# Optimization experiments

Measured on AMD Instinct MI355X. Metric: run time of the kernel, lower is better.

## Reference

```python
import jax, jax.numpy as jnp
import numpy as np

D = 512
NH = 8
DH = D // NH
B, L = 16, 1024


def setup_inputs() -> dict:
    key = jax.random.key(0)
    k1, k2, k3, k4 = jax.random.split(key, 4)
    queries = jax.random.normal(k1, (B, D, L), dtype=jnp.float32)
    mask = jax.random.randint(k2, (B, L), 0, 2, dtype=jnp.int32)
    # xavier-ish scale for 1x1 conv weights [out, in]
    w_mem = jax.random.normal(k3, (2 * D, D), dtype=jnp.float32) * (1.0 / np.sqrt(D))
    w_q = jax.random.normal(k4, (D, D), dtype=jnp.float32) * (1.0 / np.sqrt(D))
    return {"queries": queries, "mask": mask, "w_mem": w_mem, "w_q": w_q}


def _split_heads(x):
    # [B, L, D] -> [B, NH, L, DH]
    b, l, _ = x.shape
    return x.reshape(b, l, NH, DH).transpose(0, 2, 1, 3)


def reference(queries, mask, w_mem, w_q):
    # queries: [B, D, L] channels-first (1x1 Conv1d == per-position matmul)
    x = queries.transpose(0, 2, 1)                       # [B, L, D]
    mem = jnp.einsum('bld,ed->ble', x, w_mem)            # [B, L, 2D]
    qry = jnp.einsum('bld,ed->ble', x, w_q)              # [B, L, D]
    q = _split_heads(qry) * (DH ** -0.5)                 # [B, NH, L, DH]
    k = _split_heads(mem[..., :D])
    v = _split_heads(mem[..., D:])
    logits = jnp.einsum('bhqd,bhkd->bhqk', q, k)         # [B, NH, L, L]
    maskf = mask.astype(jnp.float32)[:, None, None, :]   # [B,1,1,L]
    logits = logits + (-1e30) * (1.0 - maskf)
    weights = jax.nn.softmax(logits, axis=-1)
    out = jnp.einsum('bhqk,bhkd->bhqd', weights, v)      # [B, NH, L, DH]
    out = out.transpose(0, 2, 1, 3).reshape(B, L, D)     # combine heads
    return out.transpose(0, 2, 1)                        # [B, D, L]
```

## Files before the change

kernel.cpp:

```cpp
#include <hip/hip_runtime.h>
#include <hip/hip_bf16.h>
#include <stdint.h>

#define Bsz 16
#define NHn 8
#define Dm  512
#define DHd 64
#define Ls  1024

typedef __attribute__((ext_vector_type(8))) short bf16x8;
typedef __attribute__((ext_vector_type(4))) float f32x4;
typedef __attribute__((ext_vector_type(16))) float f32x16;
typedef __attribute__((ext_vector_type(4))) unsigned int u32x4;

#define MFMA16 __builtin_amdgcn_mfma_f32_16x16x32_bf16
#define MFMA32 __builtin_amdgcn_mfma_f32_32x32x16_bf16

#define QSCALE 0.18033688011112042f

static __device__ __forceinline__ unsigned short f2bf(float f) {
    unsigned int u = __builtin_bit_cast(unsigned int, f);
    u += 0x7FFFu + ((u >> 16) & 1u);
    return (unsigned short)(u >> 16);
}

static __device__ __forceinline__ void gl2lds16(const void* g, void* l) {
    __builtin_amdgcn_global_load_lds(
        (const __attribute__((address_space(1))) unsigned int*)g,
        (__attribute__((address_space(3))) unsigned int*)l, 16, 0, 0);
}

__global__ void __launch_bounds__(256) pack_x(const float* __restrict__ q,
                                              unsigned short* __restrict__ X) {
    __shared__ float tile[64][68];
    const int bid = blockIdx.x;
    const int b  = bid >> 7;
    const int dt = (bid >> 4) & 7;
    const int lt = bid & 15;
    const int t  = threadIdx.x;
    const int tr = t >> 4;
    const int tc = (t & 15) * 4;
    const float* src = q + ((size_t)b * Dm + dt * 64) * Ls + lt * 64;
#pragma unroll
    for (int p = 0; p < 4; ++p) {
        const int r = p * 16 + tr;
        const float4 v = *(const float4*)(src + (size_t)r * Ls + tc);
        tile[r][tc+0] = v.x; tile[r][tc+1] = v.y; tile[r][tc+2] = v.z; tile[r][tc+3] = v.w;
    }
    __syncthreads();
    unsigned short* dst = X + (size_t)(b * Ls + lt * 64) * Dm + dt * 64;
#pragma unroll
    for (int p = 0; p < 4; ++p) {
        const int lr = p * 16 + tr;
        ushort4 o;
        o.x = f2bf(tile[tc+0][lr]);
        o.y = f2bf(tile[tc+1][lr]);
        o.z = f2bf(tile[tc+2][lr]);
        o.w = f2bf(tile[tc+3][lr]);
        *(ushort4*)(dst + (size_t)lr * Dm + tc) = o;
    }
}

__global__ void __launch_bounds__(256) pack_w(const float* __restrict__ wm,
                                              const float* __restrict__ wq,
                                              unsigned short* __restrict__ W) {
    const int i = (blockIdx.x * 256 + threadIdx.x) * 4;
    const int n = i >> 9;
    const int k = i & 511;
    const float* src = (n < 512) ? (wq + (size_t)n * 512 + k)
                                 : (wm + (size_t)(n - 512) * 512 + k);
    const float4 v = *(const float4*)src;
    ushort4 o;
    o.x = f2bf(v.x); o.y = f2bf(v.y); o.z = f2bf(v.z); o.w = f2bf(v.w);
    *(ushort4*)(W + i) = o;
}

__global__ void __launch_bounds__(256) gemm_qkv(const unsigned short* __restrict__ X,
                                                const unsigned short* __restrict__ W,
                                                unsigned short* __restrict__ Qb,
                                                unsigned short* __restrict__ Kb,
                                                unsigned short* __restrict__ VT) {
    __shared__ unsigned short Alds[2][128 * 64];
    __shared__ unsigned short Blds[2][128 * 64];
    const int bid = (blockIdx.x & 7) * 192 + (blockIdx.x >> 3);
    const int nt = bid % 12, mt = bid / 12;
    const int m0 = mt * 128, n0 = nt * 128;
    const int t = threadIdx.x;
    const int w = t >> 6, lane = t & 63, g = lane >> 4, c = lane & 15;
    const int wm = w >> 1, wn = w & 1;
    const int lrow = lane >> 3;
    const int scol = ((lane & 7) ^ lrow) * 8;

    const f32x4 fzero = {0.f, 0.f, 0.f, 0.f};
    f32x4 acc[4][4];
#pragma unroll
    for (int i = 0; i < 4; ++i)
#pragma unroll
        for (int j = 0; j < 4; ++j) acc[i][j] = fzero;

#define STAGE(BUF, KT) do {                                                      \
        const int k0_ = (KT) * 64;                                               \
        _Pragma("unroll")                                                        \
        for (int i_ = 0; i_ < 4; ++i_) {                                         \
            const int r0_ = w * 32 + i_ * 8;                                     \
            gl2lds16(X + (size_t)(m0 + r0_ + lrow) * Dm + k0_ + scol,            \
                     &Alds[BUF][r0_ * 64]);                                      \
            gl2lds16(W + (size_t)(n0 + r0_ + lrow) * Dm + k0_ + scol,            \
                     &Blds[BUF][r0_ * 64]);                                      \
        }                                                                        \
    } while (0)

#define KLOOP(SWAPPED) do {                                                      \
    for (int kt = 0; kt < 8; ++kt) {                                             \
        const int buf = kt & 1;                                                  \
        if (kt < 7) {                                                            \
            STAGE(buf ^ 1, kt + 1);                                              \
            asm volatile("s_waitcnt vmcnt(8)" ::: "memory");                     \
        } else {                                                                 \
            asm volatile("s_waitcnt vmcnt(0)" ::: "memory");                     \
        }                                                                        \
        __syncthreads();                                                         \
        const char* Ab = (const char*)&Alds[buf][0];                             \
        const char* Bb = (const char*)&Blds[buf][0];                             \
        _Pragma("unroll")                                                        \
        for (int kk = 0; kk < 2; ++kk) {                                         \
            bf16x8 av[4], bv[4];                                                 \
            _Pragma("unroll")                                                    \
            for (int mi = 0; mi < 4; ++mi) {                                     \
                const int R = wm * 64 + mi * 16 + c;                             \
                av[mi] = *(const bf16x8*)(Ab + R * 128 +                         \
                          ((kk * 64 + g * 16) ^ ((R & 7) << 4)));                \
            }                                                                    \
            _Pragma("unroll")                                                    \
            for (int nj = 0; nj < 4; ++nj) {                                     \
                const int R = wn * 64 + nj * 16 + c;                             \
                bv[nj] = *(const bf16x8*)(Bb + R * 128 +                         \
                          ((kk * 64 + g * 16) ^ ((R & 7) << 4)));                \
            }                                                                    \
            _Pragma("unroll")                                                    \
            for (int mi = 0; mi < 4; ++mi)                                       \
                _Pragma("unroll")                                                \
                for (int nj = 0; nj < 4; ++nj)                                   \
                    acc[mi][nj] = (SWAPPED)                                      \
                        ? MFMA16(bv[nj], av[mi], acc[mi][nj], 0, 0, 0)           \
                        : MFMA16(av[mi], bv[nj], acc[mi][nj], 0, 0, 0);          \
        }                                                                        \
        __syncthreads();                                                         \
    }                                                                            \
} while (0)

    STAGE(0, 0);
    const int bq = m0 >> 10;

    if (n0 < 1024) {
        KLOOP(1);
        const int m_loc = (m0 & 1023) + wm * 64 + c;
        const int hbase = ((n0 < 512) ? n0 : (n0 - 512)) >> 6;
        unsigned short* dstbase = (n0 < 512) ? Qb : Kb;
        const float scale = (n0 < 512) ? QSCALE : 1.0f;
        unsigned short* base = dstbase + ((size_t)(bq * NHn + hbase + wn) * Ls) * DHd;
        const int dh0 = g * 4;
#pragma unroll
        for (int nj = 0; nj < 4; ++nj) {
#pragma unroll
            for (int mi = 0; mi < 4; ++mi) {
                ushort4 o;
                o.x = f2bf(acc[mi][nj][0] * scale);
                o.y = f2bf(acc[mi][nj][1] * scale);
                o.z = f2bf(acc[mi][nj][2] * scale);
                o.w = f2bf(acc[mi][nj][3] * scale);
                *(ushort4*)(base + (size_t)(m_loc + mi * 16) * DHd + nj * 16 + dh0) = o;
            }
        }
    } else {
        KLOOP(0);
        const int m_loc = (m0 & 1023) + wm * 64 + g * 4;
        const int hbase = (n0 - 1024) >> 6;
        unsigned short* base = VT + ((size_t)(bq * NHn + hbase + wn) * DHd) * Ls;
#pragma unroll
        for (int nj = 0; nj < 4; ++nj) {
            const int dh = nj * 16 + c;
#pragma unroll
            for (int mi = 0; mi < 4; ++mi) {
                ushort4 o;
                o.x = f2bf(acc[mi][nj][0]);
                o.y = f2bf(acc[mi][nj][1]);
                o.z = f2bf(acc[mi][nj][2]);
                o.w = f2bf(acc[mi][nj][3]);
                *(ushort4*)(base + (size_t)dh * Ls + m_loc + mi * 16) = o;
            }
        }
    }
#undef KLOOP
#undef STAGE
}

__global__ void __launch_bounds__(256) attn(const unsigned short* __restrict__ Qb,
                                            const unsigned short* __restrict__ Kb,
                                            const unsigned short* __restrict__ VT,
                                            const int* __restrict__ mask,
                                            float* __restrict__ out) {
    __shared__ unsigned short Klds[2][4096];
    __shared__ unsigned short Vlds[2][4096];
    __shared__ float Mlds[1024];

    const int bid = blockIdx.x;
    const int xcd = bid & 7;
    const int idx = bid >> 3;
    const int qblk = idx & 7;
    const int bh = ((idx >> 3) << 3) | xcd;
    const int b = bh >> 3, h = bh & 7;
    const int t = threadIdx.x, w = t >> 6, lane = t & 63;
    const int c5 = lane & 31, hi = lane >> 5;
    const int sw = (c5 & 7) << 4;

    const unsigned short* Qh = Qb + (size_t)bh * (Ls * DHd);
    const unsigned short* Kh = Kb + (size_t)bh * (Ls * DHd);
    const unsigned short* Vh = VT + (size_t)bh * (DHd * Ls);
    const int q = qblk * 128 + w * 32 + c5;

    {
        const int4 mv = *(const int4*)(mask + b * Ls + t * 4);
        Mlds[t*4+0] = mv.x ? 0.f : -1e30f;
        Mlds[t*4+1] = mv.y ? 0.f : -1e30f;
        Mlds[t*4+2] = mv.z ? 0.f : -1e30f;
        Mlds[t*4+3] = mv.w ? 0.f : -1e30f;
    }

    bf16x8 qf[4];
#pragma unroll
    for (int ks = 0; ks < 4; ++ks)
        qf[ks] = *(const bf16x8*)(Qh + (size_t)q * DHd + ks * 16 + hi * 8);

    const int r0 = t >> 3,        c0b = (t & 7) << 4;
    const int r1 = (t + 256) >> 3, c1b = ((t + 256) & 7) << 4;
    const int ksrc0 = r0 * 128  + (c0b ^ ((r0 & 7) << 4));
    const int ksrc1 = r1 * 128  + (c1b ^ ((r1 & 7) << 4));
    const int vsrc0 = r0 * 2048 + (c0b ^ ((r0 & 7) << 4));
    const int vsrc1 = r1 * 2048 + (c1b ^ ((r1 & 7) << 4));

#define STAGE(BUF, KV0) do {                                          \
        const char* Kc = (const char*)Kh + (size_t)(KV0) * 128;       \
        const char* Vc = (const char*)Vh + (size_t)(KV0) * 2;         \
        gl2lds16(Kc + ksrc0, &Klds[BUF][w * 512]);                    \
        gl2lds16(Kc + ksrc1, &Klds[BUF][2048 + w * 512]);             \
        gl2lds16(Vc + vsrc0, &Vlds[BUF][w * 512]);                    \
        gl2lds16(Vc + vsrc1, &Vlds[BUF][2048 + w * 512]);             \
    } while (0)

    STAGE(0, 0);

    float lsum = 0.f;
    f32x16 oacc0, oacc1;
#pragma unroll
    for (int i = 0; i < 16; ++i) { oacc0[i] = 0.f; oacc1[i] = 0.f; }

    for (int it = 0; it < 16; ++it) {
        const int kv0 = it * 64;
        const int buf = it & 1;
        asm volatile("s_waitcnt vmcnt(0)" ::: "memory");
        __syncthreads();
        if (it < 15) STAGE(buf ^ 1, kv0 + 64);

        f32x16 acc0, acc1;
#pragma unroll
        for (int u = 0; u < 4; ++u) {
            const float4 m0 = *(const float4*)&Mlds[kv0 + u * 8 + hi * 4];
            acc0[4*u+0] = m0.x; acc0[4*u+1] = m0.y; acc0[4*u+2] = m0.z; acc0[4*u+3] = m0.w;
            const float4 m1 = *(const float4*)&Mlds[kv0 + 32 + u * 8 + hi * 4];
            acc1[4*u+0] = m1.x; acc1[4*u+1] = m1.y; acc1[4*u+2] = m1.z; acc1[4*u+3] = m1.w;
        }

        const char* Kbase = (const char*)&Klds[buf][0];
#pragma unroll
        for (int ks = 0; ks < 4; ++ks) {
            const bf16x8 k0 = *(const bf16x8*)(Kbase + c5 * 128 + ((ks * 32 + hi * 16) ^ sw));
            acc0 = MFMA32(k0, qf[ks], acc0, 0, 0, 0);
            const bf16x8 k1 = *(const bf16x8*)(Kbase + (32 + c5) * 128 + ((ks * 32 + hi * 16) ^ sw));
            acc1 = MFMA32(k1, qf[ks], acc1, 0, 0, 0);
        }

        unsigned pk0[8], pk1[8];
#pragma unroll
        for (int u = 0; u < 4; ++u) {
            float p0 = __builtin_amdgcn_exp2f(acc0[4*u+0]);
            float p1 = __builtin_amdgcn_exp2f(acc0[4*u+1]);
            float p2 = __builtin_amdgcn_exp2f(acc0[4*u+2]);
            float p3 = __builtin_amdgcn_exp2f(acc0[4*u+3]);
            lsum += (p0 + p1) + (p2 + p3);
            asm("v_cvt_pk_bf16_f32 %0, %1, %2" : "=v"(pk0[2*u+0]) : "v"(p0), "v"(p1));
            asm("v_cvt_pk_bf16_f32 %0, %1, %2" : "=v"(pk0[2*u+1]) : "v"(p2), "v"(p3));
            float s0 = __builtin_amdgcn_exp2f(acc1[4*u+0]);
            float s1 = __builtin_amdgcn_exp2f(acc1[4*u+1]);
            float s2 = __builtin_amdgcn_exp2f(acc1[4*u+2]);
            float s3 = __builtin_amdgcn_exp2f(acc1[4*u+3]);
            lsum += (s0 + s1) + (s2 + s3);
            asm("v_cvt_pk_bf16_f32 %0, %1, %2" : "=v"(pk1[2*u+0]) : "v"(s0), "v"(s1));
            asm("v_cvt_pk_bf16_f32 %0, %1, %2" : "=v"(pk1[2*u+1]) : "v"(s2), "v"(s3));
        }

        const char* Vbase = (const char*)&Vlds[buf][0];
#define PV_STEP(S, PK) do {                                                         \
            unsigned a0 = PK[2 * (2 * ((S) & 1) + 0) + 0];                          \
            unsigned a1 = PK[2 * (2 * ((S) & 1) + 0) + 1];                          \
            unsigned b0 = PK[2 * (2 * ((S) & 1) + 1) + 0];                          \
            unsigned b1 = PK[2 * (2 * ((S) & 1) + 1) + 1];                          \
            asm("v_permlane32_swap_b32 %0, %1" : "+v"(a0), "+v"(b0));               \
            asm("v_permlane32_swap_b32 %0, %1" : "+v"(a1), "+v"(b1));               \
            const u32x4 fw = {a0, a1, b0, b1};                                      \
            const bf16x8 pf = __builtin_bit_cast(bf16x8, fw);                       \
            const bf16x8 v0 = *(const bf16x8*)(Vbase + c5 * 128 + (((S) * 32 + hi * 16) ^ sw)); \
            oacc0 = MFMA32(v0, pf, oacc0, 0, 0, 0);                                 \
            const bf16x8 v1 = *(const bf16x8*)(Vbase + (32 + c5) * 128 + (((S) * 32 + hi * 16) ^ sw)); \
            oacc1 = MFMA32(v1, pf, oacc1, 0, 0, 0);                                 \
        } while (0)
        PV_STEP(0, pk0);
        PV_STEP(1, pk0);
        PV_STEP(2, pk1);
        PV_STEP(3, pk1);
#undef PV_STEP
    }

    lsum += __shfl_xor(lsum, 32);
    const float rinv = __builtin_amdgcn_rcpf(lsum);
    float* ob = out + (size_t)(b * Dm + h * DHd) * Ls + q;
#pragma unroll
    for (int reg = 0; reg < 16; ++reg) {
        const int dh = (reg & 3) + 8 * (reg >> 2) + 4 * hi;
        ob[(size_t)dh * Ls] = oacc0[reg] * rinv;
    }
#pragma unroll
    for (int reg = 0; reg < 16; ++reg) {
        const int dh = 32 + (reg & 3) + 8 * (reg >> 2) + 4 * hi;
        ob[(size_t)dh * Ls] = oacc1[reg] * rinv;
    }
#undef STAGE
}

extern "C" void kernel_launch(void* const* d_in, const int* in_sizes, int n_in,
                              void* d_out, int out_size, void* d_ws, size_t ws_size,
                              hipStream_t stream) {
    const float* queries = (const float*)d_in[0];
    const int*   mask    = (const int*)d_in[1];
    const float* w_mem   = (const float*)d_in[2];
    const float* w_q     = (const float*)d_in[3];
    float* out = (float*)d_out;

    char* ws = (char*)d_ws;
    unsigned short* X  = (unsigned short*)(ws);
    unsigned short* W  = (unsigned short*)(ws + 16777216);
    unsigned short* Qb = (unsigned short*)(ws + 18350080);
    unsigned short* Kb = (unsigned short*)(ws + 35127296);
    unsigned short* VT = (unsigned short*)(ws + 51904512);
    if (ws_size < 68681728) return;

    pack_x<<<dim3(2048), dim3(256), 0, stream>>>(queries, X);
    pack_w<<<dim3(768),  dim3(256), 0, stream>>>(w_mem, w_q, W);
    gemm_qkv<<<dim3(1536), dim3(256), 0, stream>>>(X, W, Qb, Kb, VT);
    attn<<<dim3(1024), dim3(256), 0, stream>>>(Qb, Kb, VT, mask, out);
}
```

Baseline: 101.6 us.

## Fold key mask into K/V projection epilogue and correct softmax denominator

The QKV GEMM epilogue now writes zeros for K rows and V columns at masked key positions. Masked logits therefore become 0, so each masked key adds exp2(0)=1 to the row sum and nothing to the output. The attention kernel drops the per-iteration mask bias loads from LDS and the mask LDS buffer. Instead it counts masked keys once per block and subtracts that count from the softmax denominator. This removes LDS traffic and accumulator initialisation from the inner loop, at the cost of extra mask reads in the GEMM epilogue and a small rounding change in the row sum.

```diff
diff --git a/kernel.cpp b/kernel.cpp
--- a/kernel.cpp
+++ b/kernel.cpp
@@ -77,6 +77,7 @@
 
 __global__ void __launch_bounds__(256) gemm_qkv(const unsigned short* __restrict__ X,
                                                 const unsigned short* __restrict__ W,
+                                                const int* __restrict__ mask,
                                                 unsigned short* __restrict__ Qb,
                                                 unsigned short* __restrict__ Kb,
                                                 unsigned short* __restrict__ VT) {
@@ -156,19 +157,28 @@
         KLOOP(1);
         const int m_loc = (m0 & 1023) + wm * 64 + c;
         const int hbase = ((n0 < 512) ? n0 : (n0 - 512)) >> 6;
-        unsigned short* dstbase = (n0 < 512) ? Qb : Kb;
-        const float scale = (n0 < 512) ? QSCALE : 1.0f;
+        const bool isK = (n0 >= 512);
+        unsigned short* dstbase = isK ? Kb : Qb;
+        const float scale = isK ? 1.0f : QSCALE;
         unsigned short* base = dstbase + ((size_t)(bq * NHn + hbase + wn) * Ls) * DHd;
         const int dh0 = g * 4;
+        int mk[4];
+#pragma unroll
+        for (int mi = 0; mi < 4; ++mi)
+            mk[mi] = isK ? mask[bq * Ls + m_loc + mi * 16] : 1;
 #pragma unroll
         for (int nj = 0; nj < 4; ++nj) {
 #pragma unroll
             for (int mi = 0; mi < 4; ++mi) {
                 ushort4 o;
-                o.x = f2bf(acc[mi][nj][0] * scale);
-                o.y = f2bf(acc[mi][nj][1] * scale);
-                o.z = f2bf(acc[mi][nj][2] * scale);
-                o.w = f2bf(acc[mi][nj][3] * scale);
+                if (mk[mi]) {
+                    o.x = f2bf(acc[mi][nj][0] * scale);
+                    o.y = f2bf(acc[mi][nj][1] * scale);
+                    o.z = f2bf(acc[mi][nj][2] * scale);
+                    o.w = f2bf(acc[mi][nj][3] * scale);
+                } else {
+                    o.x = 0; o.y = 0; o.z = 0; o.w = 0;
+                }
                 *(ushort4*)(base + (size_t)(m_loc + mi * 16) * DHd + nj * 16 + dh0) = o;
             }
         }
@@ -177,16 +187,20 @@
         const int m_loc = (m0 & 1023) + wm * 64 + g * 4;
         const int hbase = (n0 - 1024) >> 6;
         unsigned short* base = VT + ((size_t)(bq * NHn + hbase + wn) * DHd) * Ls;
+        int4 mv[4];
+#pragma unroll
+        for (int mi = 0; mi < 4; ++mi)
+            mv[mi] = *(const int4*)(mask + bq * Ls + m_loc + mi * 16);
 #pragma unroll
         for (int nj = 0; nj < 4; ++nj) {
             const int dh = nj * 16 + c;
 #pragma unroll
             for (int mi = 0; mi < 4; ++mi) {
                 ushort4 o;
-                o.x = f2bf(acc[mi][nj][0]);
-                o.y = f2bf(acc[mi][nj][1]);
-                o.z = f2bf(acc[mi][nj][2]);
-                o.w = f2bf(acc[mi][nj][3]);
+                o.x = mv[mi].x ? f2bf(acc[mi][nj][0]) : (unsigned short)0;
+                o.y = mv[mi].y ? f2bf(acc[mi][nj][1]) : (unsigned short)0;
+                o.z = mv[mi].z ? f2bf(acc[mi][nj][2]) : (unsigned short)0;
+                o.w = mv[mi].w ? f2bf(acc[mi][nj][3]) : (unsigned short)0;
                 *(ushort4*)(base + (size_t)dh * Ls + m_loc + mi * 16) = o;
             }
         }
@@ -202,7 +216,6 @@
                                             float* __restrict__ out) {
     __shared__ unsigned short Klds[2][4096];
     __shared__ unsigned short Vlds[2][4096];
-    __shared__ float Mlds[1024];
 
     const int bid = blockIdx.x;
     const int xcd = bid & 7;
@@ -219,12 +232,18 @@
     const unsigned short* Vh = VT + (size_t)bh * (DHd * Ls);
     const int q = qblk * 128 + w * 32 + c5;
 
+    float fnmask;
     {
-        const int4 mv = *(const int4*)(mask + b * Ls + t * 4);
-        Mlds[t*4+0] = mv.x ? 0.f : -1e30f;
-        Mlds[t*4+1] = mv.y ? 0.f : -1e30f;
-        Mlds[t*4+2] = mv.z ? 0.f : -1e30f;
-        Mlds[t*4+3] = mv.w ? 0.f : -1e30f;
+        int s = 0;
+        const int4* mp = (const int4*)(mask + b * Ls);
+#pragma unroll
+        for (int j = 0; j < 4; ++j) {
+            const int4 mv = mp[j * 64 + lane];
+            s += (mv.x + mv.y) + (mv.z + mv.w);
+        }
+#pragma unroll
+        for (int off = 1; off < 64; off <<= 1) s += __shfl_xor(s, off);
+        fnmask = (float)(Ls - s);
     }
 
     bf16x8 qf[4];
@@ -264,12 +283,7 @@
 
         f32x16 acc0, acc1;
 #pragma unroll
-        for (int u = 0; u < 4; ++u) {
-            const float4 m0 = *(const float4*)&Mlds[kv0 + u * 8 + hi * 4];
-            acc0[4*u+0] = m0.x; acc0[4*u+1] = m0.y; acc0[4*u+2] = m0.z; acc0[4*u+3] = m0.w;
-            const float4 m1 = *(const float4*)&Mlds[kv0 + 32 + u * 8 + hi * 4];
-            acc1[4*u+0] = m1.x; acc1[4*u+1] = m1.y; acc1[4*u+2] = m1.z; acc1[4*u+3] = m1.w;
-        }
+        for (int i = 0; i < 16; ++i) { acc0[i] = 0.f; acc1[i] = 0.f; }
 
         const char* Kbase = (const char*)&Klds[buf][0];
 #pragma unroll
@@ -322,6 +336,7 @@
     }
 
     lsum += __shfl_xor(lsum, 32);
+    lsum -= fnmask;
     const float rinv = __builtin_amdgcn_rcpf(lsum);
     float* ob = out + (size_t)(b * Dm + h * DHd) * Ls + q;
 #pragma unroll
@@ -356,6 +371,6 @@
 
     pack_x<<<dim3(2048), dim3(256), 0, stream>>>(queries, X);
     pack_w<<<dim3(768),  dim3(256), 0, stream>>>(w_mem, w_q, W);
-    gemm_qkv<<<dim3(1536), dim3(256), 0, stream>>>(X, W, Qb, Kb, VT);
+    gemm_qkv<<<dim3(1536), dim3(256), 0, stream>>>(X, W, mask, Qb, Kb, VT);
     attn<<<dim3(1024), dim3(256), 0, stream>>>(Qb, Kb, VT, mask, out);
 }
```

Result: no change. 102.7 us (median of 4 runs) (+1.1%).
